# Kernel optimization log

Hardware: AMD Instinct MI355X
Metric: run time of the kernel (lower is better)

Reference implementation:

```python
import jax, jax.numpy as jnp
import numpy as np

N = 50000      # nodes
E_BASE = 400000  # random edges (avg degree 8)
E = E_BASE + N   # + self loops (added by add_self_loops in the torch code)
D = 128        # in_channels == hidden_output


def gcn_conv(x, src, dst, w, W, b, n_nodes):
    """PyG GCNConv with precomputed self-loops: h = x@W + b; symmetric-norm scatter-add."""
    h = x @ W + b                                            # [N, H]
    deg = jax.ops.segment_sum(w, dst, num_segments=n_nodes)  # weighted in-degree
    dinv = jnp.where(deg > 0, jax.lax.rsqrt(deg), 0.0)
    norm = dinv[src] * w * dinv[dst]                         # [E]
    msg = h[src] * norm[:, None]                             # gather + scale
    return jax.ops.segment_sum(msg, dst, num_segments=n_nodes)


def prelu(z, alpha):
    return jnp.where(z >= 0, z, alpha[None, :] * z)


def gconv(x, src, dst, w, W1, b1, W2, b2, alpha, n_nodes):
    z = prelu(gcn_conv(x, src, dst, w, W1, b1, n_nodes), alpha)
    z = prelu(gcn_conv(z, src, dst, w, W2, b2, n_nodes), alpha)
    return z


def setup_inputs() -> dict:
    key = jax.random.key(0)
    ks = jax.random.split(key, 12)
    src = jax.random.randint(ks[0], (E_BASE,), 0, N)
    dst = jax.random.randint(ks[1], (E_BASE,), 0, N)
    loops = jnp.arange(N, dtype=src.dtype)
    edge_index = jnp.stack([jnp.concatenate([src, loops]),
                            jnp.concatenate([dst, loops])])
    # |time_encoder| output used as edge weight -> positive; self-loop fill_value=1.0
    edge_weight = jnp.concatenate([
        jax.random.uniform(ks[2], (E_BASE,), minval=0.1, maxval=1.0),
        jnp.ones((N,), jnp.float32)])
    x = jax.random.normal(ks[3], (N, D), jnp.float32)
    s = 1.0 / np.sqrt(D)
    def lin(k):
        return jax.random.uniform(k, (D, D), jnp.float32, -s, s)
    return {
        "x": x, "edge_index": edge_index, "edge_weight": edge_weight,
        "perm1": jax.random.permutation(ks[4], N),
        "perm2": jax.random.permutation(ks[5], N),
        "W1a": lin(ks[6]), "b1a": jnp.zeros((D,), jnp.float32),
        "W2a": lin(ks[7]), "b2a": jnp.zeros((D,), jnp.float32),
        "alpha1": jnp.full((D,), 0.25, jnp.float32),
        "W1b": lin(ks[8]), "b1b": jnp.zeros((D,), jnp.float32),
        "W2b": lin(ks[9]), "b2b": jnp.zeros((D,), jnp.float32),
        "alpha2": jnp.full((D,), 0.25, jnp.float32),
        "projW": lin(ks[10]), "projb": jnp.zeros((D,), jnp.float32),
    }


def reference(x, edge_index, edge_weight, perm1, perm2,
              W1a, b1a, W2a, b2a, alpha1,
              W1b, b1b, W2b, b2b, alpha2, projW, projb):
    src, dst = edge_index[0], edge_index[1]
    n = x.shape[0]
    # two views (Identity augmentors), two encoders
    z1 = gconv(x, src, dst, edge_weight, W1a, b1a, W2a, b2a, alpha1, n)
    z2 = gconv(x, src, dst, edge_weight, W1b, b1b, W2b, b2b, alpha2, n)
    g1 = jax.nn.sigmoid(z1.mean(axis=0, keepdims=True)) @ projW + projb  # [1, H]
    g2 = jax.nn.sigmoid(z2.mean(axis=0, keepdims=True)) @ projW + projb
    # corruption: permute node features, keep graph structure
    z1n = gconv(x[perm1], src, dst, edge_weight, W1a, b1a, W2a, b2a, alpha1, n)
    z2n = gconv(x[perm2], src, dst, edge_weight, W1b, b1b, W2b, b2b, alpha2, n)
    return (z1, z2, g1, g2, z1n, z2n)
```

## Files before the change

kernel.cpp:

```cpp
#include <hip/hip_runtime.h>
#include <math.h>

#define D 128

typedef __attribute__((ext_vector_type(8))) short bf16x8;
typedef __attribute__((ext_vector_type(4))) float f32x4;

__device__ __forceinline__ unsigned short f2bf(float f) {
  unsigned u = __float_as_uint(f);
  unsigned r = (u + 0x7fffu + ((u >> 16) & 1u)) >> 16;
  return (unsigned short)r;
}
__device__ __forceinline__ unsigned pack2bf(float x, float y) {
  return (unsigned)f2bf(x) | ((unsigned)f2bf(y) << 16);
}
__device__ __forceinline__ float bf_lo(unsigned u) { return __uint_as_float(u << 16); }
__device__ __forceinline__ float bf_hi(unsigned u) { return __uint_as_float(u & 0xffff0000u); }


__global__ __launch_bounds__(256) void hist_k(const int* __restrict__ dst,
    const float* __restrict__ w, float* __restrict__ deg,
    int* __restrict__ cnt, int E) {
  int e = blockIdx.x * 256 + threadIdx.x;
  if (e < E) {
    int d = dst[e];
    atomicAdd(&deg[d], w[e]);
    atomicAdd(&cnt[d], 1);
  }
}

__global__ __launch_bounds__(256) void scan1_k(const int* __restrict__ cnt,
    int* __restrict__ offs, int* __restrict__ bsum, int n) {
  __shared__ int ls[256];
  int t = threadIdx.x;
  int base = blockIdx.x * 1024 + t * 4;
  int v0 = 0, v1 = 0, v2 = 0, v3 = 0;
  if (base + 0 < n) v0 = cnt[base + 0];
  if (base + 1 < n) v1 = cnt[base + 1];
  if (base + 2 < n) v2 = cnt[base + 2];
  if (base + 3 < n) v3 = cnt[base + 3];
  int s = v0 + v1 + v2 + v3;
  ls[t] = s;
  __syncthreads();
  for (int off = 1; off < 256; off <<= 1) {
    int x = 0;
    if (t >= off) x = ls[t - off];
    __syncthreads();
    if (t >= off) ls[t] += x;
    __syncthreads();
  }
  int run = (t > 0) ? ls[t - 1] : 0;
  if (base + 0 < n) offs[base + 0] = run; run += v0;
  if (base + 1 < n) offs[base + 1] = run; run += v1;
  if (base + 2 < n) offs[base + 2] = run; run += v2;
  if (base + 3 < n) offs[base + 3] = run;
  if (t == 255) bsum[blockIdx.x] = ls[255];
}

__global__ void scan2_k(int* bsum, int nb) {
  if (threadIdx.x == 0) {
    int run = 0;
    for (int i = 0; i < nb; ++i) { int v = bsum[i]; bsum[i] = run; run += v; }
  }
}

__global__ __launch_bounds__(256) void scan3_k(int* __restrict__ offs,
    const int* __restrict__ bsum, int n, int total) {
  int t = threadIdx.x;
  int add = bsum[blockIdx.x];
  int base = blockIdx.x * 1024 + t * 4;
#pragma unroll
  for (int i = 0; i < 4; ++i)
    if (base + i < n) offs[base + i] += add;
  if (blockIdx.x == 0 && t == 0) offs[n] = total;
}

__global__ __launch_bounds__(256) void fillnorm_k(const int* __restrict__ src,
    const int* __restrict__ dst, const float* __restrict__ w,
    const float* __restrict__ deg, const int* __restrict__ perm1,
    const int* __restrict__ perm2, const int* __restrict__ offs,
    int* __restrict__ cur, int2* __restrict__ ep, int2* __restrict__ pp, int E) {
  int e = blockIdx.x * 256 + threadIdx.x;
  if (e >= E) return;
  int s = src[e], d = dst[e];
  float ds = deg[s], dd = deg[d];
  float a = ds > 0.f ? rsqrtf(ds) : 0.f;
  float b = dd > 0.f ? rsqrtf(dd) : 0.f;
  float nr = a * w[e] * b;
  int p = atomicAdd(&cur[d], 1);
  int pos = offs[d] + p;
  ep[pos] = make_int2(s, __float_as_int(nr));
  pp[pos] = make_int2(perm1[s], perm2[s]);
}


__global__ __launch_bounds__(256) void prep_k(const float* __restrict__ x,
    const float* __restrict__ W1a, const float* __restrict__ W2a,
    const float* __restrict__ W1b, const float* __restrict__ W2b,
    unsigned short* __restrict__ xb,
    unsigned short* __restrict__ F1a, unsigned short* __restrict__ F2a,
    unsigned short* __restrict__ F1b, unsigned short* __restrict__ F2b, int n) {
  int b = blockIdx.x, t = threadIdx.x;
  if (b < 32) {
    const float* Wsrc = (b < 8) ? W1a : (b < 16) ? W2a : (b < 24) ? W1b : W2b;
    unsigned short* Fdst = (b < 8) ? F1a : (b < 16) ? F2a : (b < 24) ? F1b : F2b;
    int u = ((b & 7) << 8) + t;
    int l = u & 63;
    int ct = (u >> 6) & 7;
    int kk5 = u >> 9;
    int nn = (ct << 4) + (l & 15);
    int kb = (kk5 << 5) + ((l >> 4) << 3);
    unsigned r0 = pack2bf(Wsrc[(kb + 0) * D + nn], Wsrc[(kb + 1) * D + nn]);
    unsigned r1 = pack2bf(Wsrc[(kb + 2) * D + nn], Wsrc[(kb + 3) * D + nn]);
    unsigned r2 = pack2bf(Wsrc[(kb + 4) * D + nn], Wsrc[(kb + 5) * D + nn]);
    unsigned r3 = pack2bf(Wsrc[(kb + 6) * D + nn], Wsrc[(kb + 7) * D + nn]);
    ((uint4*)Fdst)[u] = make_uint4(r0, r1, r2, r3);
  } else {
    size_t i = (size_t)(b - 32) * 256 + t;
    size_t total = (size_t)n * (D / 8);
    if (i < total) {
      const float4* xs = (const float4*)x;
      float4 a = xs[i * 2], c = xs[i * 2 + 1];
      ((uint4*)xb)[i] = make_uint4(pack2bf(a.x, a.y), pack2bf(a.z, a.w),
                                   pack2bf(c.x, c.y), pack2bf(c.z, c.w));
    }
  }
}


struct GemmArgs {
  const unsigned short* A[4];
  const unsigned short* W[4];
  const float* bias[4];
  unsigned short* out[4];
};

__global__ __launch_bounds__(256) void gemm_k(GemmArgs ga, int n) {
  int y = blockIdx.y;
  const unsigned short* A = ga.A[y];
  const unsigned short* Wf = ga.W[y];
  const float* bias = ga.bias[y];
  unsigned short* outb = ga.out[y];

  __shared__ __attribute__((aligned(16))) unsigned short Wl[16384];
  int t = threadIdx.x;
  {
    const uint4* srcp = (const uint4*)Wf;
    uint4* dstp = (uint4*)Wl;
#pragma unroll
    for (int i = 0; i < 8; ++i) dstp[t + (i << 8)] = srcp[t + (i << 8)];
  }
  __syncthreads();
  int wave = t >> 6, lane = t & 63;
  int row0 = (blockIdx.x << 6) + (wave << 4);
  int r = row0 + (lane & 15);
  int kg = (lane >> 4) << 3;
  f32x4 acc[8];
#pragma unroll
  for (int ct = 0; ct < 8; ++ct) {
    float bv = bias[(ct << 4) + (lane & 15)];
    acc[ct] = (f32x4){bv, bv, bv, bv};
  }
  bool inb = (r < n);
  const bf16x8* Wlv = (const bf16x8*)Wl;
#pragma unroll
  for (int ks = 0; ks < 4; ++ks) {
    bf16x8 a = {0, 0, 0, 0, 0, 0, 0, 0};
    if (inb) a = *(const bf16x8*)(A + (size_t)r * D + (ks << 5) + kg);
#pragma unroll
    for (int ct = 0; ct < 8; ++ct) {
      bf16x8 bb = Wlv[((ks << 3) + ct) * 64 + lane];
      acc[ct] = __builtin_amdgcn_mfma_f32_16x16x32_bf16(a, bb, acc[ct], 0, 0, 0);
    }
  }
  int orow = row0 + ((lane >> 4) << 2);
#pragma unroll
  for (int ct = 0; ct < 8; ++ct) {
    int col = (ct << 4) + (lane & 15);
#pragma unroll
    for (int v = 0; v < 4; ++v) {
      int rr = orow + v;
      if (rr < n) outb[(size_t)rr * D + col] = f2bf(acc[ct][v]);
    }
  }
}


template <bool FINAL>
__global__ __launch_bounds__(256) void agg4_k(
    const unsigned* __restrict__ T0, const unsigned* __restrict__ T1,
    const unsigned* __restrict__ T2, const unsigned* __restrict__ T3,
    const int2* __restrict__ ep, const int2* __restrict__ pp,
    const int* __restrict__ offs,
    const float* __restrict__ al1, const float* __restrict__ al2,
    unsigned* __restrict__ O0b, unsigned* __restrict__ O1b,
    unsigned* __restrict__ O2b, unsigned* __restrict__ O3b,
    float* __restrict__ O0f, float* __restrict__ O1f,
    float* __restrict__ O2f, float* __restrict__ O3f,
    float* __restrict__ csum, int n) {
  int wave = threadIdx.x >> 6, lane = threadIdx.x & 63;
  int node = blockIdx.x * 4 + wave;
  float2 a0 = make_float2(0.f, 0.f), a1 = make_float2(0.f, 0.f);
  float2 a2 = make_float2(0.f, 0.f), a3 = make_float2(0.f, 0.f);

  if (node < n) {
    int beg = offs[node], end = offs[node + 1];
    int j = beg;
    for (; j + 4 <= end; j += 4) {
      unsigned g0[4], g1[4], g2[4], g3[4];
      float nr[4];
#pragma unroll
      for (int u = 0; u < 4; ++u) {
        int2 e = ep[j + u];
        nr[u] = __int_as_float(e.y);
        int s = e.x, ia = s, ib = s;
        if constexpr (!FINAL) {
          int2 q = pp[j + u];
          ia = q.x; ib = q.y;
        }
        g0[u] = T0[(size_t)s * 64 + lane];
        g1[u] = T1[(size_t)ia * 64 + lane];
        g2[u] = T2[(size_t)s * 64 + lane];
        g3[u] = T3[(size_t)ib * 64 + lane];
      }
#pragma unroll
      for (int u = 0; u < 4; ++u) {
        a0.x = fmaf(bf_lo(g0[u]), nr[u], a0.x); a0.y = fmaf(bf_hi(g0[u]), nr[u], a0.y);
        a1.x = fmaf(bf_lo(g1[u]), nr[u], a1.x); a1.y = fmaf(bf_hi(g1[u]), nr[u], a1.y);
        a2.x = fmaf(bf_lo(g2[u]), nr[u], a2.x); a2.y = fmaf(bf_hi(g2[u]), nr[u], a2.y);
        a3.x = fmaf(bf_lo(g3[u]), nr[u], a3.x); a3.y = fmaf(bf_hi(g3[u]), nr[u], a3.y);
      }
    }
    for (; j < end; ++j) {
      int2 e = ep[j];
      float nu = __int_as_float(e.y);
      int s = e.x, ia = s, ib = s;
      if constexpr (!FINAL) {
        int2 q = pp[j];
        ia = q.x; ib = q.y;
      }
      unsigned u0 = T0[(size_t)s * 64 + lane];
      unsigned u1 = T1[(size_t)ia * 64 + lane];
      unsigned u2 = T2[(size_t)s * 64 + lane];
      unsigned u3 = T3[(size_t)ib * 64 + lane];
      a0.x = fmaf(bf_lo(u0), nu, a0.x); a0.y = fmaf(bf_hi(u0), nu, a0.y);
      a1.x = fmaf(bf_lo(u1), nu, a1.x); a1.y = fmaf(bf_hi(u1), nu, a1.y);
      a2.x = fmaf(bf_lo(u2), nu, a2.x); a2.y = fmaf(bf_hi(u2), nu, a2.y);
      a3.x = fmaf(bf_lo(u3), nu, a3.x); a3.y = fmaf(bf_hi(u3), nu, a3.y);
    }
  }

  float2 alA = ((const float2*)al1)[lane];
  float2 alB = ((const float2*)al2)[lane];
  float2 o0 = make_float2(0.f, 0.f), o1 = o0, o2 = o0, o3 = o0;
  if (node < n) {
    o0.x = a0.x >= 0.f ? a0.x : alA.x * a0.x;  o0.y = a0.y >= 0.f ? a0.y : alA.y * a0.y;
    o1.x = a1.x >= 0.f ? a1.x : alA.x * a1.x;  o1.y = a1.y >= 0.f ? a1.y : alA.y * a1.y;
    o2.x = a2.x >= 0.f ? a2.x : alB.x * a2.x;  o2.y = a2.y >= 0.f ? a2.y : alB.y * a2.y;
    o3.x = a3.x >= 0.f ? a3.x : alB.x * a3.x;  o3.y = a3.y >= 0.f ? a3.y : alB.y * a3.y;
    size_t idx = (size_t)node * 64 + lane;
    if constexpr (FINAL) {
      ((float2*)O0f)[idx] = o0;
      ((float2*)O1f)[idx] = o1;
      ((float2*)O2f)[idx] = o2;
      ((float2*)O3f)[idx] = o3;
    } else {
      O0b[idx] = pack2bf(o0.x, o0.y);
      O1b[idx] = pack2bf(o1.x, o1.y);
      O2b[idx] = pack2bf(o2.x, o2.y);
      O3b[idx] = pack2bf(o3.x, o3.y);
    }
  }

  if constexpr (FINAL) {
    __shared__ float2 red[2][4][64];
    red[0][wave][lane] = o0;
    red[1][wave][lane] = o2;
    __syncthreads();
    if (wave < 2) {
      float2 s0 = red[wave][0][lane], s1 = red[wave][1][lane];
      float2 s2 = red[wave][2][lane], s3 = red[wave][3][lane];
      float sx = s0.x + s1.x + s2.x + s3.x;
      float sy = s0.y + s1.y + s2.y + s3.y;
      float* base = csum + wave * 4096 + (blockIdx.x & 31) * 128;
      atomicAdd(&base[2 * lane], sx);
      atomicAdd(&base[2 * lane + 1], sy);
    }
  }
}


__global__ __launch_bounds__(128) void proj_k(const float* __restrict__ csum,
    const float* __restrict__ pW, const float* __restrict__ pb,
    float* __restrict__ g, float invN) {
  __shared__ float sg[128];
  int t = threadIdx.x;
  float s = 0.f;
#pragma unroll
  for (int i = 0; i < 32; ++i) s += csum[i * 128 + t];
  sg[t] = 1.f / (1.f + expf(-s * invN));
  __syncthreads();
  float a = pb[t];
  for (int k = 0; k < 128; ++k)
    a = fmaf(sg[k], pW[k * 128 + t], a);
  g[t] = a;
}


extern "C" void kernel_launch(void* const* d_in, const int* in_sizes, int n_in,
                              void* d_out, int out_size, void* d_ws, size_t ws_size,
                              hipStream_t stream) {
  const float* x   = (const float*)d_in[0];
  const int*   ei  = (const int*)d_in[1];
  const float* w   = (const float*)d_in[2];
  const int* perm1 = (const int*)d_in[3];
  const int* perm2 = (const int*)d_in[4];
  const float* W1a = (const float*)d_in[5];
  const float* b1a = (const float*)d_in[6];
  const float* W2a = (const float*)d_in[7];
  const float* b2a = (const float*)d_in[8];
  const float* al1 = (const float*)d_in[9];
  const float* W1b = (const float*)d_in[10];
  const float* b1b = (const float*)d_in[11];
  const float* W2b = (const float*)d_in[12];
  const float* b2b = (const float*)d_in[13];
  const float* al2 = (const float*)d_in[14];
  const float* pW  = (const float*)d_in[15];
  const float* pb  = (const float*)d_in[16];

  const int E = in_sizes[2];
  const int N = in_sizes[3];
  const int* srcA = ei;
  const int* dstA = ei + E;

  float* out = (float*)d_out;
  size_t ND = (size_t)N * D;
  float* z1  = out;
  float* z2  = out + ND;
  float* g1  = out + 2 * ND;
  float* g2  = g1 + D;
  float* z1n = g2 + D;
  float* z2n = z1n + ND;

  char* p = (char*)d_ws;
  auto carve = [&](size_t bytes) {
    char* r = p;
    p += (bytes + 255) & ~(size_t)255;
    return r;
  };
  float* deg  = (float*)carve((size_t)N * 4);
  int*   cnt  = (int*)carve((size_t)N * 4);
  int*   cur  = (int*)carve((size_t)N * 4);
  size_t zeroBytes = (size_t)((char*)(cur + N) - (char*)deg);
  int*   offs = (int*)carve((size_t)(N + 1) * 4);
  int*   bsum = (int*)carve(256 * 4);
  int2*  ep   = (int2*)carve((size_t)E * 8);
  int2*  pp   = (int2*)carve((size_t)E * 8);
  unsigned short* xb  = (unsigned short*)carve(ND * 2);
  unsigned short* h1a = (unsigned short*)carve(ND * 2);
  unsigned short* h1b = (unsigned short*)carve(ND * 2);
  unsigned short* yx  = (unsigned short*)carve(ND * 2);
  unsigned short* F1a = (unsigned short*)carve(32768);
  unsigned short* F2a = (unsigned short*)carve(32768);
  unsigned short* F1b = (unsigned short*)carve(32768);
  unsigned short* F2b = (unsigned short*)carve(32768);
  float* csum = (float*)carve(2 * 32 * 128 * 4);

  unsigned* mAa = (unsigned*)z1n;
  unsigned* mPa = (unsigned*)z1n + ND / 2;
  unsigned* mAb = (unsigned*)z2n;
  unsigned* mPb = (unsigned*)z2n + ND / 2;

  int nbE = (E + 255) / 256;
  int nbS = (N + 1023) / 1024;
  int nbA = (N + 3) / 4;
  int nbG = (N + 63) / 64;
  int nbP = 32 + (int)(((size_t)N * (D / 8) + 255) / 256);

  prep_k<<<nbP, 256, 0, stream>>>(x, W1a, W2a, W1b, W2b, xb, F1a, F2a, F1b, F2b, N);
  hipMemsetAsync(deg, 0, zeroBytes, stream);
  hipMemsetAsync(csum, 0, 2 * 32 * 128 * 4, stream);
  hist_k<<<nbE, 256, 0, stream>>>(dstA, w, deg, cnt, E);
  scan1_k<<<nbS, 256, 0, stream>>>(cnt, offs, bsum, N);
  scan2_k<<<1, 64, 0, stream>>>(bsum, nbS);
  scan3_k<<<nbS, 256, 0, stream>>>(offs, bsum, N, E);
  fillnorm_k<<<nbE, 256, 0, stream>>>(srcA, dstA, w, deg, perm1, perm2, offs,
                                      cur, ep, pp, E);

  GemmArgs g1a;
  g1a.A[0] = xb;  g1a.W[0] = F1a; g1a.bias[0] = b1a; g1a.out[0] = h1a;
  g1a.A[1] = xb;  g1a.W[1] = F1b; g1a.bias[1] = b1b; g1a.out[1] = h1b;
  g1a.A[2] = xb;  g1a.W[2] = F1a; g1a.bias[2] = b1a; g1a.out[2] = h1a;
  g1a.A[3] = xb;  g1a.W[3] = F1a; g1a.bias[3] = b1a; g1a.out[3] = h1a;
  gemm_k<<<dim3(nbG, 2), 256, 0, stream>>>(g1a, N);

  agg4_k<false><<<nbA, 256, 0, stream>>>(
      (const unsigned*)h1a, (const unsigned*)h1a,
      (const unsigned*)h1b, (const unsigned*)h1b,
      ep, pp, offs, al1, al2,
      mAa, mPa, mAb, mPb,
      nullptr, nullptr, nullptr, nullptr, nullptr, N);

  GemmArgs g2a;
  g2a.A[0] = (const unsigned short*)mAa; g2a.W[0] = F2a; g2a.bias[0] = b2a; g2a.out[0] = xb;
  g2a.A[1] = (const unsigned short*)mPa; g2a.W[1] = F2a; g2a.bias[1] = b2a; g2a.out[1] = h1a;
  g2a.A[2] = (const unsigned short*)mAb; g2a.W[2] = F2b; g2a.bias[2] = b2b; g2a.out[2] = h1b;
  g2a.A[3] = (const unsigned short*)mPb; g2a.W[3] = F2b; g2a.bias[3] = b2b; g2a.out[3] = yx;
  gemm_k<<<dim3(nbG, 4), 256, 0, stream>>>(g2a, N);

  agg4_k<true><<<nbA, 256, 0, stream>>>(
      (const unsigned*)xb, (const unsigned*)h1a,
      (const unsigned*)h1b, (const unsigned*)yx,
      ep, nullptr, offs, al1, al2,
      nullptr, nullptr, nullptr, nullptr,
      z1, z1n, z2, z2n, csum, N);

  float invN = 1.0f / (float)N;
  proj_k<<<1, 128, 0, stream>>>(csum, pW, pb, g1, invN);
  proj_k<<<1, 128, 0, stream>>>(csum + 4096, pW, pb, g2, invN);
}
```

Measured before the change: 288.0 us.

## Interleave GEMM outputs so aggregation gathers multiple views per row

After: 304.0 us (median of 5 runs). 5.5% more time.

```diff
diff --git a/kernel.cpp b/kernel.cpp
--- a/kernel.cpp
+++ b/kernel.cpp
@@ -16,6 +16,10 @@
 }
 __device__ __forceinline__ float bf_lo(unsigned u) { return __uint_as_float(u << 16); }
 __device__ __forceinline__ float bf_hi(unsigned u) { return __uint_as_float(u & 0xffff0000u); }
+
+__device__ __forceinline__ int colmap(int ct, int j) {
+  return 2 * (((ct >> 1) << 4) + j) + (ct & 1);
+}
 
 
 __global__ __launch_bounds__(256) void hist_k(const int* __restrict__ dst,
@@ -108,7 +112,7 @@
     int l = u & 63;
     int ct = (u >> 6) & 7;
     int kk5 = u >> 9;
-    int nn = (ct << 4) + (l & 15);
+    int nn = colmap(ct, l & 15);
     int kb = (kk5 << 5) + ((l >> 4) << 3);
     unsigned r0 = pack2bf(Wsrc[(kb + 0) * D + nn], Wsrc[(kb + 1) * D + nn]);
     unsigned r1 = pack2bf(Wsrc[(kb + 2) * D + nn], Wsrc[(kb + 3) * D + nn]);
@@ -128,164 +132,268 @@
 }
 
 
-struct GemmArgs {
-  const unsigned short* A[4];
-  const unsigned short* W[4];
-  const float* bias[4];
-  unsigned short* out[4];
-};
-
-__global__ __launch_bounds__(256) void gemm_k(GemmArgs ga, int n) {
-  int y = blockIdx.y;
-  const unsigned short* A = ga.A[y];
-  const unsigned short* Wf = ga.W[y];
-  const float* bias = ga.bias[y];
-  unsigned short* outb = ga.out[y];
-
-  __shared__ __attribute__((aligned(16))) unsigned short Wl[16384];
+__global__ __launch_bounds__(256) void gemm1_k(const unsigned short* __restrict__ A,
+    const unsigned short* __restrict__ Fa, const unsigned short* __restrict__ Fb,
+    const float* __restrict__ ba, const float* __restrict__ bb,
+    unsigned* __restrict__ h1aT, unsigned* __restrict__ h1bT,
+    uint2* __restrict__ hAB, int n) {
+  __shared__ __attribute__((aligned(16))) unsigned short Wl[2][16384];
   int t = threadIdx.x;
   {
-    const uint4* srcp = (const uint4*)Wf;
-    uint4* dstp = (uint4*)Wl;
-#pragma unroll
-    for (int i = 0; i < 8; ++i) dstp[t + (i << 8)] = srcp[t + (i << 8)];
+    const uint4* sa = (const uint4*)Fa;
+    const uint4* sb = (const uint4*)Fb;
+    uint4* da = (uint4*)Wl[0];
+    uint4* db = (uint4*)Wl[1];
+#pragma unroll
+    for (int i = 0; i < 8; ++i) { da[t + (i << 8)] = sa[t + (i << 8)]; db[t + (i << 8)] = sb[t + (i << 8)]; }
   }
   __syncthreads();
   int wave = t >> 6, lane = t & 63;
   int row0 = (blockIdx.x << 6) + (wave << 4);
   int r = row0 + (lane & 15);
   int kg = (lane >> 4) << 3;
-  f32x4 acc[8];
+  f32x4 accA[8], accB[8];
 #pragma unroll
   for (int ct = 0; ct < 8; ++ct) {
-    float bv = bias[(ct << 4) + (lane & 15)];
-    acc[ct] = (f32x4){bv, bv, bv, bv};
+    int col = colmap(ct, lane & 15);
+    float bva = ba[col], bvb = bb[col];
+    accA[ct] = (f32x4){bva, bva, bva, bva};
+    accB[ct] = (f32x4){bvb, bvb, bvb, bvb};
   }
   bool inb = (r < n);
-  const bf16x8* Wlv = (const bf16x8*)Wl;
+  const bf16x8* WA = (const bf16x8*)Wl[0];
+  const bf16x8* WB = (const bf16x8*)Wl[1];
 #pragma unroll
   for (int ks = 0; ks < 4; ++ks) {
     bf16x8 a = {0, 0, 0, 0, 0, 0, 0, 0};
     if (inb) a = *(const bf16x8*)(A + (size_t)r * D + (ks << 5) + kg);
 #pragma unroll
     for (int ct = 0; ct < 8; ++ct) {
-      bf16x8 bb = Wlv[((ks << 3) + ct) * 64 + lane];
-      acc[ct] = __builtin_amdgcn_mfma_f32_16x16x32_bf16(a, bb, acc[ct], 0, 0, 0);
+      bf16x8 wa = WA[((ks << 3) + ct) * 64 + lane];
+      bf16x8 wb = WB[((ks << 3) + ct) * 64 + lane];
+      accA[ct] = __builtin_amdgcn_mfma_f32_16x16x32_bf16(a, wa, accA[ct], 0, 0, 0);
+      accB[ct] = __builtin_amdgcn_mfma_f32_16x16x32_bf16(a, wb, accB[ct], 0, 0, 0);
     }
   }
   int orow = row0 + ((lane >> 4) << 2);
 #pragma unroll
-  for (int ct = 0; ct < 8; ++ct) {
-    int col = (ct << 4) + (lane & 15);
+  for (int m = 0; m < 4; ++m) {
+    int cp = (m << 4) + (lane & 15);
 #pragma unroll
     for (int v = 0; v < 4; ++v) {
       int rr = orow + v;
-      if (rr < n) outb[(size_t)rr * D + col] = f2bf(acc[ct][v]);
-    }
-  }
-}
-
-
-template <bool FINAL>
-__global__ __launch_bounds__(256) void agg4_k(
-    const unsigned* __restrict__ T0, const unsigned* __restrict__ T1,
-    const unsigned* __restrict__ T2, const unsigned* __restrict__ T3,
+      if (rr < n) {
+        unsigned pa = pack2bf(accA[2 * m][v], accA[2 * m + 1][v]);
+        unsigned pb = pack2bf(accB[2 * m][v], accB[2 * m + 1][v]);
+        size_t idx = (size_t)rr * 64 + cp;
+        h1aT[idx] = pa;
+        h1bT[idx] = pb;
+        hAB[idx] = make_uint2(pa, pb);
+      }
+    }
+  }
+}
+
+
+__global__ __launch_bounds__(256) void gemm2_k(
+    const unsigned short* __restrict__ A0, const unsigned short* __restrict__ A1,
+    const unsigned short* __restrict__ A2, const unsigned short* __restrict__ A3,
+    const unsigned short* __restrict__ Fa, const unsigned short* __restrict__ Fb,
+    const float* __restrict__ ba, const float* __restrict__ bb,
+    uint4* __restrict__ t4, int n) {
+  __shared__ __attribute__((aligned(16))) unsigned short Wl[2][16384];
+  int t = threadIdx.x;
+  {
+    const uint4* sa = (const uint4*)Fa;
+    const uint4* sb = (const uint4*)Fb;
+    uint4* da = (uint4*)Wl[0];
+    uint4* db = (uint4*)Wl[1];
+#pragma unroll
+    for (int i = 0; i < 8; ++i) { da[t + (i << 8)] = sa[t + (i << 8)]; db[t + (i << 8)] = sb[t + (i << 8)]; }
+  }
+  __syncthreads();
+  int wave = t >> 6, lane = t & 63;
+  int row0 = (blockIdx.x << 6) + (wave << 4);
+  int r = row0 + (lane & 15);
+  int kg = (lane >> 4) << 3;
+  f32x4 acc0[8], acc1[8], acc2[8], acc3[8];
+#pragma unroll
+  for (int ct = 0; ct < 8; ++ct) {
+    int col = colmap(ct, lane & 15);
+    float bva = ba[col], bvb = bb[col];
+    acc0[ct] = (f32x4){bva, bva, bva, bva};
+    acc1[ct] = (f32x4){bva, bva, bva, bva};
+    acc2[ct] = (f32x4){bvb, bvb, bvb, bvb};
+    acc3[ct] = (f32x4){bvb, bvb, bvb, bvb};
+  }
+  bool inb = (r < n);
+  const bf16x8* WA = (const bf16x8*)Wl[0];
+  const bf16x8* WB = (const bf16x8*)Wl[1];
+#pragma unroll
+  for (int ks = 0; ks < 4; ++ks) {
+    bf16x8 a0 = {0,0,0,0,0,0,0,0}, a1 = a0, a2 = a0, a3 = a0;
+    if (inb) {
+      size_t off = (size_t)r * D + (ks << 5) + kg;
+      a0 = *(const bf16x8*)(A0 + off);
+      a1 = *(const bf16x8*)(A1 + off);
+      a2 = *(const bf16x8*)(A2 + off);
+      a3 = *(const bf16x8*)(A3 + off);
+    }
+#pragma unroll
+    for (int ct = 0; ct < 8; ++ct) {
+      bf16x8 wa = WA[((ks << 3) + ct) * 64 + lane];
+      bf16x8 wb = WB[((ks << 3) + ct) * 64 + lane];
+      acc0[ct] = __builtin_amdgcn_mfma_f32_16x16x32_bf16(a0, wa, acc0[ct], 0, 0, 0);
+      acc1[ct] = __builtin_amdgcn_mfma_f32_16x16x32_bf16(a1, wa, acc1[ct], 0, 0, 0);
+      acc2[ct] = __builtin_amdgcn_mfma_f32_16x16x32_bf16(a2, wb, acc2[ct], 0, 0, 0);
+      acc3[ct] = __builtin_amdgcn_mfma_f32_16x16x32_bf16(a3, wb, acc3[ct], 0, 0, 0);
+    }
+  }
+  int orow = row0 + ((lane >> 4) << 2);
+#pragma unroll
+  for (int m = 0; m < 4; ++m) {
+    int cp = (m << 4) + (lane & 15);
+#pragma unroll
+    for (int v = 0; v < 4; ++v) {
+      int rr = orow + v;
+      if (rr < n) {
+        uint4 q;
+        q.x = pack2bf(acc0[2 * m][v], acc0[2 * m + 1][v]);
+        q.y = pack2bf(acc1[2 * m][v], acc1[2 * m + 1][v]);
+        q.z = pack2bf(acc2[2 * m][v], acc2[2 * m + 1][v]);
+        q.w = pack2bf(acc3[2 * m][v], acc3[2 * m + 1][v]);
+        t4[(size_t)rr * 64 + cp] = q;
+      }
+    }
+  }
+}
+
+
+__global__ __launch_bounds__(256) void aggL_k(
+    const uint2* __restrict__ hAB, const unsigned* __restrict__ h1aT,
+    const unsigned* __restrict__ h1bT,
     const int2* __restrict__ ep, const int2* __restrict__ pp,
     const int* __restrict__ offs,
     const float* __restrict__ al1, const float* __restrict__ al2,
-    unsigned* __restrict__ O0b, unsigned* __restrict__ O1b,
-    unsigned* __restrict__ O2b, unsigned* __restrict__ O3b,
-    float* __restrict__ O0f, float* __restrict__ O1f,
-    float* __restrict__ O2f, float* __restrict__ O3f,
+    unsigned* __restrict__ O0, unsigned* __restrict__ O1,
+    unsigned* __restrict__ O2, unsigned* __restrict__ O3, int n) {
+  int wave = threadIdx.x >> 6, lane = threadIdx.x & 63;
+  int node = blockIdx.x * 4 + wave;
+  if (node >= n) return;
+  float2 a0 = make_float2(0.f, 0.f), a1 = a0, a2 = a0, a3 = a0;
+  int beg = offs[node], end = offs[node + 1];
+  int j = beg;
+  for (; j + 4 <= end; j += 4) {
+    uint2 gs[4]; unsigned g1[4], g3[4]; float nr[4];
+#pragma unroll
+    for (int u = 0; u < 4; ++u) {
+      int2 e = ep[j + u];
+      int2 q = pp[j + u];
+      nr[u] = __int_as_float(e.y);
+      gs[u] = hAB[(size_t)e.x * 64 + lane];
+      g1[u] = h1aT[(size_t)q.x * 64 + lane];
+      g3[u] = h1bT[(size_t)q.y * 64 + lane];
+    }
+#pragma unroll
+    for (int u = 0; u < 4; ++u) {
+      a0.x = fmaf(bf_lo(gs[u].x), nr[u], a0.x); a0.y = fmaf(bf_hi(gs[u].x), nr[u], a0.y);
+      a2.x = fmaf(bf_lo(gs[u].y), nr[u], a2.x); a2.y = fmaf(bf_hi(gs[u].y), nr[u], a2.y);
+      a1.x = fmaf(bf_lo(g1[u]), nr[u], a1.x);   a1.y = fmaf(bf_hi(g1[u]), nr[u], a1.y);
+      a3.x = fmaf(bf_lo(g3[u]), nr[u], a3.x);   a3.y = fmaf(bf_hi(g3[u]), nr[u], a3.y);
+    }
+  }
+  for (; j < end; ++j) {
+    int2 e = ep[j];
+    int2 q = pp[j];
+    float nu = __int_as_float(e.y);
+    uint2 gs = hAB[(size_t)e.x * 64 + lane];
+    unsigned g1v = h1aT[(size_t)q.x * 64 + lane];
+    unsigned g3v = h1bT[(size_t)q.y * 64 + lane];
+    a0.x = fmaf(bf_lo(gs.x), nu, a0.x); a0.y = fmaf(bf_hi(gs.x), nu, a0.y);
+    a2.x = fmaf(bf_lo(gs.y), nu, a2.x); a2.y = fmaf(bf_hi(gs.y), nu, a2.y);
+    a1.x = fmaf(bf_lo(g1v), nu, a1.x);  a1.y = fmaf(bf_hi(g1v), nu, a1.y);
+    a3.x = fmaf(bf_lo(g3v), nu, a3.x);  a3.y = fmaf(bf_hi(g3v), nu, a3.y);
+  }
+  float2 alA = ((const float2*)al1)[lane];
+  float2 alB = ((const float2*)al2)[lane];
+  float2 o0, o1, o2, o3;
+  o0.x = a0.x >= 0.f ? a0.x : alA.x * a0.x;  o0.y = a0.y >= 0.f ? a0.y : alA.y * a0.y;
+  o1.x = a1.x >= 0.f ? a1.x : alA.x * a1.x;  o1.y = a1.y >= 0.f ? a1.y : alA.y * a1.y;
+  o2.x = a2.x >= 0.f ? a2.x : alB.x * a2.x;  o2.y = a2.y >= 0.f ? a2.y : alB.y * a2.y;
+  o3.x = a3.x >= 0.f ? a3.x : alB.x * a3.x;  o3.y = a3.y >= 0.f ? a3.y : alB.y * a3.y;
+  size_t idx = (size_t)node * 64 + lane;
+  O0[idx] = pack2bf(o0.x, o0.y);
+  O1[idx] = pack2bf(o1.x, o1.y);
+  O2[idx] = pack2bf(o2.x, o2.y);
+  O3[idx] = pack2bf(o3.x, o3.y);
+}
+
+
+__global__ __launch_bounds__(256) void aggF_k(const uint4* __restrict__ t4,
+    const int2* __restrict__ ep, const int* __restrict__ offs,
+    const float* __restrict__ al1, const float* __restrict__ al2,
+    float* __restrict__ O0, float* __restrict__ O1,
+    float* __restrict__ O2, float* __restrict__ O3,
     float* __restrict__ csum, int n) {
   int wave = threadIdx.x >> 6, lane = threadIdx.x & 63;
   int node = blockIdx.x * 4 + wave;
-  float2 a0 = make_float2(0.f, 0.f), a1 = make_float2(0.f, 0.f);
-  float2 a2 = make_float2(0.f, 0.f), a3 = make_float2(0.f, 0.f);
-
+  float2 a0 = make_float2(0.f, 0.f), a1 = a0, a2 = a0, a3 = a0;
   if (node < n) {
     int beg = offs[node], end = offs[node + 1];
     int j = beg;
-    for (; j + 4 <= end; j += 4) {
-      unsigned g0[4], g1[4], g2[4], g3[4];
-      float nr[4];
-#pragma unroll
-      for (int u = 0; u < 4; ++u) {
+    for (; j + 8 <= end; j += 8) {
+      uint4 g[8]; float nr[8];
+#pragma unroll
+      for (int u = 0; u < 8; ++u) {
         int2 e = ep[j + u];
         nr[u] = __int_as_float(e.y);
-        int s = e.x, ia = s, ib = s;
-        if constexpr (!FINAL) {
-          int2 q = pp[j + u];
-          ia = q.x; ib = q.y;
-        }
-        g0[u] = T0[(size_t)s * 64 + lane];
-        g1[u] = T1[(size_t)ia * 64 + lane];
-        g2[u] = T2[(size_t)s * 64 + lane];
-        g3[u] = T3[(size_t)ib * 64 + lane];
+        g[u] = t4[(size_t)e.x * 64 + lane];
       }
 #pragma unroll
-      for (int u = 0; u < 4; ++u) {
-        a0.x = fmaf(bf_lo(g0[u]), nr[u], a0.x); a0.y = fmaf(bf_hi(g0[u]), nr[u], a0.y);
-        a1.x = fmaf(bf_lo(g1[u]), nr[u], a1.x); a1.y = fmaf(bf_hi(g1[u]), nr[u], a1.y);
-        a2.x = fmaf(bf_lo(g2[u]), nr[u], a2.x); a2.y = fmaf(bf_hi(g2[u]), nr[u], a2.y);
-        a3.x = fmaf(bf_lo(g3[u]), nr[u], a3.x); a3.y = fmaf(bf_hi(g3[u]), nr[u], a3.y);
+      for (int u = 0; u < 8; ++u) {
+        a0.x = fmaf(bf_lo(g[u].x), nr[u], a0.x); a0.y = fmaf(bf_hi(g[u].x), nr[u], a0.y);
+        a1.x = fmaf(bf_lo(g[u].y), nr[u], a1.x); a1.y = fmaf(bf_hi(g[u].y), nr[u], a1.y);
+        a2.x = fmaf(bf_lo(g[u].z), nr[u], a2.x); a2.y = fmaf(bf_hi(g[u].z), nr[u], a2.y);
+        a3.x = fmaf(bf_lo(g[u].w), nr[u], a3.x); a3.y = fmaf(bf_hi(g[u].w), nr[u], a3.y);
       }
     }
     for (; j < end; ++j) {
       int2 e = ep[j];
       float nu = __int_as_float(e.y);
-      int s = e.x, ia = s, ib = s;
-      if constexpr (!FINAL) {
-        int2 q = pp[j];
-        ia = q.x; ib = q.y;
-      }
-      unsigned u0 = T0[(size_t)s * 64 + lane];
-      unsigned u1 = T1[(size_t)ia * 64 + lane];
-      unsigned u2 = T2[(size_t)s * 64 + lane];
-      unsigned u3 = T3[(size_t)ib * 64 + lane];
-      a0.x = fmaf(bf_lo(u0), nu, a0.x); a0.y = fmaf(bf_hi(u0), nu, a0.y);
-      a1.x = fmaf(bf_lo(u1), nu, a1.x); a1.y = fmaf(bf_hi(u1), nu, a1.y);
-      a2.x = fmaf(bf_lo(u2), nu, a2.x); a2.y = fmaf(bf_hi(u2), nu, a2.y);
-      a3.x = fmaf(bf_lo(u3), nu, a3.x); a3.y = fmaf(bf_hi(u3), nu, a3.y);
-    }
-  }
-
+      uint4 g = t4[(size_t)e.x * 64 + lane];
+      a0.x = fmaf(bf_lo(g.x), nu, a0.x); a0.y = fmaf(bf_hi(g.x), nu, a0.y);
+      a1.x = fmaf(bf_lo(g.y), nu, a1.x); a1.y = fmaf(bf_hi(g.y), nu, a1.y);
+      a2.x = fmaf(bf_lo(g.z), nu, a2.x); a2.y = fmaf(bf_hi(g.z), nu, a2.y);
+      a3.x = fmaf(bf_lo(g.w), nu, a3.x); a3.y = fmaf(bf_hi(g.w), nu, a3.y);
+    }
+  }
   float2 alA = ((const float2*)al1)[lane];
   float2 alB = ((const float2*)al2)[lane];
-  float2 o0 = make_float2(0.f, 0.f), o1 = o0, o2 = o0, o3 = o0;
+  float2 o0 = make_float2(0.f, 0.f), o2 = o0;
   if (node < n) {
+    float2 o1, o3;
     o0.x = a0.x >= 0.f ? a0.x : alA.x * a0.x;  o0.y = a0.y >= 0.f ? a0.y : alA.y * a0.y;
     o1.x = a1.x >= 0.f ? a1.x : alA.x * a1.x;  o1.y = a1.y >= 0.f ? a1.y : alA.y * a1.y;
     o2.x = a2.x >= 0.f ? a2.x : alB.x * a2.x;  o2.y = a2.y >= 0.f ? a2.y : alB.y * a2.y;
     o3.x = a3.x >= 0.f ? a3.x : alB.x * a3.x;  o3.y = a3.y >= 0.f ? a3.y : alB.y * a3.y;
     size_t idx = (size_t)node * 64 + lane;
-    if constexpr (FINAL) {
-      ((float2*)O0f)[idx] = o0;
-      ((float2*)O1f)[idx] = o1;
-      ((float2*)O2f)[idx] = o2;
-      ((float2*)O3f)[idx] = o3;
-    } else {
-      O0b[idx] = pack2bf(o0.x, o0.y);
-      O1b[idx] = pack2bf(o1.x, o1.y);
-      O2b[idx] = pack2bf(o2.x, o2.y);
-      O3b[idx] = pack2bf(o3.x, o3.y);
-    }
-  }
-
-  if constexpr (FINAL) {
-    __shared__ float2 red[2][4][64];
-    red[0][wave][lane] = o0;
-    red[1][wave][lane] = o2;
-    __syncthreads();
-    if (wave < 2) {
-      float2 s0 = red[wave][0][lane], s1 = red[wave][1][lane];
-      float2 s2 = red[wave][2][lane], s3 = red[wave][3][lane];
-      float sx = s0.x + s1.x + s2.x + s3.x;
-      float sy = s0.y + s1.y + s2.y + s3.y;
-      float* base = csum + wave * 4096 + (blockIdx.x & 31) * 128;
-      atomicAdd(&base[2 * lane], sx);
-      atomicAdd(&base[2 * lane + 1], sy);
-    }
+    ((float2*)O0)[idx] = o0;
+    ((float2*)O1)[idx] = o1;
+    ((float2*)O2)[idx] = o2;
+    ((float2*)O3)[idx] = o3;
+  }
+  __shared__ float2 red[2][4][64];
+  red[0][wave][lane] = o0;
+  red[1][wave][lane] = o2;
+  __syncthreads();
+  if (wave < 2) {
+    float2 s0 = red[wave][0][lane], s1 = red[wave][1][lane];
+    float2 s2 = red[wave][2][lane], s3 = red[wave][3][lane];
+    float sx = s0.x + s1.x + s2.x + s3.x;
+    float sy = s0.y + s1.y + s2.y + s3.y;
+    float* base = csum + wave * 4096 + (blockIdx.x & 31) * 128;
+    atomicAdd(&base[2 * lane], sx);
+    atomicAdd(&base[2 * lane + 1], sy);
   }
 }
 
@@ -356,15 +464,18 @@
   int*   bsum = (int*)carve(256 * 4);
   int2*  ep   = (int2*)carve((size_t)E * 8);
   int2*  pp   = (int2*)carve((size_t)E * 8);
-  unsigned short* xb  = (unsigned short*)carve(ND * 2);
-  unsigned short* h1a = (unsigned short*)carve(ND * 2);
-  unsigned short* h1b = (unsigned short*)carve(ND * 2);
-  unsigned short* yx  = (unsigned short*)carve(ND * 2);
+  char*  big  = carve(ND * 8);
+  unsigned* h1aT = (unsigned*)big;
+  unsigned* h1bT = (unsigned*)(big + ND * 2);
+  uint2*    hAB  = (uint2*)(big + ND * 4);
+  uint4*    t4   = (uint4*)big;
   unsigned short* F1a = (unsigned short*)carve(32768);
   unsigned short* F2a = (unsigned short*)carve(32768);
   unsigned short* F1b = (unsigned short*)carve(32768);
   unsigned short* F2b = (unsigned short*)carve(32768);
   float* csum = (float*)carve(2 * 32 * 128 * 4);
+
+  unsigned short* xb = (unsigned short*)z1;
 
   unsigned* mAa = (unsigned*)z1n;
   unsigned* mPa = (unsigned*)z1n + ND / 2;
@@ -387,33 +498,18 @@
   fillnorm_k<<<nbE, 256, 0, stream>>>(srcA, dstA, w, deg, perm1, perm2, offs,
                                       cur, ep, pp, E);
 
-  GemmArgs g1a;
-  g1a.A[0] = xb;  g1a.W[0] = F1a; g1a.bias[0] = b1a; g1a.out[0] = h1a;
-  g1a.A[1] = xb;  g1a.W[1] = F1b; g1a.bias[1] = b1b; g1a.out[1] = h1b;
-  g1a.A[2] = xb;  g1a.W[2] = F1a; g1a.bias[2] = b1a; g1a.out[2] = h1a;
-  g1a.A[3] = xb;  g1a.W[3] = F1a; g1a.bias[3] = b1a; g1a.out[3] = h1a;
-  gemm_k<<<dim3(nbG, 2), 256, 0, stream>>>(g1a, N);
-
-  agg4_k<false><<<nbA, 256, 0, stream>>>(
-      (const unsigned*)h1a, (const unsigned*)h1a,
-      (const unsigned*)h1b, (const unsigned*)h1b,
-      ep, pp, offs, al1, al2,
-      mAa, mPa, mAb, mPb,
-      nullptr, nullptr, nullptr, nullptr, nullptr, N);
-
-  GemmArgs g2a;
-  g2a.A[0] = (const unsigned short*)mAa; g2a.W[0] = F2a; g2a.bias[0] = b2a; g2a.out[0] = xb;
-  g2a.A[1] = (const unsigned short*)mPa; g2a.W[1] = F2a; g2a.bias[1] = b2a; g2a.out[1] = h1a;
-  g2a.A[2] = (const unsigned short*)mAb; g2a.W[2] = F2b; g2a.bias[2] = b2b; g2a.out[2] = h1b;
-  g2a.A[3] = (const unsigned short*)mPb; g2a.W[3] = F2b; g2a.bias[3] = b2b; g2a.out[3] = yx;
-  gemm_k<<<dim3(nbG, 4), 256, 0, stream>>>(g2a, N);
-
-  agg4_k<true><<<nbA, 256, 0, stream>>>(
-      (const unsigned*)xb, (const unsigned*)h1a,
-      (const unsigned*)h1b, (const unsigned*)yx,
-      ep, nullptr, offs, al1, al2,
-      nullptr, nullptr, nullptr, nullptr,
-      z1, z1n, z2, z2n, csum, N);
+  gemm1_k<<<nbG, 256, 0, stream>>>(xb, F1a, F1b, b1a, b1b, h1aT, h1bT, hAB, N);
+
+  aggL_k<<<nbA, 256, 0, stream>>>(hAB, h1aT, h1bT, ep, pp, offs, al1, al2,
+                                  mAa, mPa, mAb, mPb, N);
+
+  gemm2_k<<<nbG, 256, 0, stream>>>(
+      (const unsigned short*)mAa, (const unsigned short*)mPa,
+      (const unsigned short*)mAb, (const unsigned short*)mPb,
+      F2a, F2b, b2a, b2b, t4, N);
+
+  aggF_k<<<nbA, 256, 0, stream>>>(t4, ep, offs, al1, al2,
+                                  z1, z1n, z2, z2n, csum, N);
 
   float invN = 1.0f / (float)N;
   proj_k<<<1, 128, 0, stream>>>(csum, pW, pb, g1, invN);
```
